# Kernel optimization log

Hardware: AMD Instinct MI355X
Metric: run time of the kernel (lower is better)

## Reference

```python
import jax, jax.numpy as jnp
import numpy as np

EPS = 1e-5

def _conv(x, w, b):
    # NCHW, OIHW, stride 1, SAME padding (kernel 3, padding 1)
    y = jax.lax.conv_general_dilated(x, w, (1, 1), 'SAME',
                                     dimension_numbers=('NCHW', 'OIHW', 'NCHW'))
    return y + b[None, :, None, None]

def _maxpool2(x):
    return jax.lax.reduce_window(x, -jnp.inf, jax.lax.max,
                                 (1, 1, 2, 2), (1, 1, 2, 2), 'VALID')

def _fraud_layer(v, theta, phases, sq_r, disp_r, disp_phi, kerr):
    # classical shim of a 2-mode photonic layer; all params are zero -> identity
    c, s = jnp.cos(theta), jnp.sin(theta)
    rot = jnp.array([[1.0, 0.0], [0.0, 1.0]]) * c + jnp.array([[0.0, -1.0], [1.0, 0.0]]) * s
    v = v @ rot.T
    v = v * jnp.cos(phases)          # phase shifters
    v = v * jnp.exp(sq_r)            # squeezing
    v = v + disp_r * jnp.cos(disp_phi)  # displacement
    return v + kerr * v ** 3         # Kerr nonlinearity

def setup_inputs() -> dict:
    key = jax.random.key(0)
    ks = jax.random.split(key, 16)
    B = 4096
    inp = {
        'x': jax.random.normal(ks[0], (B, 1, 32, 32), jnp.float32),
        'conv1_w': jax.random.normal(ks[1], (8, 1, 3, 3), jnp.float32) * 0.2,
        'conv1_b': jnp.zeros((8,), jnp.float32),
        'conv2_w': jax.random.normal(ks[2], (16, 8, 3, 3), jnp.float32) * 0.1,
        'conv2_b': jnp.zeros((16,), jnp.float32),
        'conv3_w': jax.random.normal(ks[3], (32, 16, 3, 3), jnp.float32) * 0.1,
        'conv3_b': jnp.zeros((32,), jnp.float32),
        'gnn_w1': jax.random.normal(ks[4], (32, 32), jnp.float32) * 0.2,
        'gnn_w2': jax.random.normal(ks[5], (16, 32), jnp.float32) * 0.2,
        'rotation_params': jax.random.normal(ks[6], (4, 4), jnp.float32),
        'entangle_params': jax.random.normal(ks[7], (3,), jnp.float32),
        'reduce_w': jax.random.normal(ks[8], (2, 32), jnp.float32) * 0.2,
        'reduce_b': jnp.zeros((2,), jnp.float32),
        'cls_w': jax.random.normal(ks[9], (2, 2), jnp.float32) * 0.5,
        'cls_b': jnp.zeros((2,), jnp.float32),
        'bn_gamma': jnp.ones((2,), jnp.float32),
        'bn_beta': jnp.zeros((2,), jnp.float32),
    }
    return inp

def reference(x, conv1_w, conv1_b, conv2_w, conv2_b, conv3_w, conv3_b,
              gnn_w1, gnn_w2, rotation_params, entangle_params,
              reduce_w, reduce_b, cls_w, cls_b, bn_gamma, bn_beta):
    B = x.shape[0]
    # CNN feature extractor
    h = jax.nn.relu(_conv(x, conv1_w, conv1_b))
    h = _maxpool2(h)
    h = jax.nn.relu(_conv(h, conv2_w, conv2_b))
    h = _maxpool2(h)
    h = jax.nn.relu(_conv(h, conv3_w, conv3_b))
    feats = jnp.mean(h, axis=(2, 3))  # AdaptiveAvgPool2d((1,1)) -> (B, 32)
    # GNN feedforward (batched equivalent of the per-sample Python loop)
    a = jnp.tanh(feats @ gnn_w1.T)    # (B, 32)
    g = jnp.tanh(a @ gnn_w2.T)        # (B, 16)
    # Quantum-style self-attention (runs on detached numpy in original -> stop_gradient)
    d = g.shape[-1]
    q = (g.reshape(B, 4, 4) @ rotation_params).reshape(B, d)
    k = (g.reshape(B, 4, 4) @ rotation_params.T).reshape(B, d)
    temp = jnp.mean(jnp.cos(entangle_params))
    logits = (q @ k.T) * (temp / jnp.sqrt(jnp.asarray(d, jnp.float32)))  # (B, B)
    attn = jax.nn.softmax(logits, axis=-1) @ g                           # (B, 16)
    rep = jnp.concatenate([g, attn], axis=-1)                            # (B, 32)
    rep = jax.lax.stop_gradient(rep)  # numpy round-trip breaks the autograd graph
    # reduce -> fraud layers (all-zero params -> identity) -> classifier
    reduced = rep @ reduce_w.T + reduce_b  # (B, 2)
    z = jnp.zeros((2,), jnp.float32)
    for _ in range(2):  # input layer + 1 hidden layer, all-zero FraudLayerParameters
        reduced = _fraud_layer(reduced, 0.0, z, z, z, z, z)
    out = reduced @ cls_w.T + cls_b  # (B, 2)
    # BatchNorm1d(2) in training mode: batch stats, biased variance
    mu = jnp.mean(out, axis=0)
    var = jnp.mean((out - mu) ** 2, axis=0)
    out = bn_gamma * (out - mu) * jax.lax.rsqrt(var + EPS) + bn_beta
    return out
```

## Files before the change

kernel.cpp:

```cpp
#include <hip/hip_runtime.h>
#include <math.h>

#define LOG2E 1.4426950408889634f

typedef _Float16 h2v __attribute__((ext_vector_type(2)));
typedef _Float16 h4  __attribute__((ext_vector_type(4)));
typedef _Float16 h8  __attribute__((ext_vector_type(8)));
typedef float    f4  __attribute__((ext_vector_type(4)));

__device__ __forceinline__ h2v pk(float a, float b) {
    return __builtin_bit_cast(h2v, __builtin_amdgcn_cvt_pkrtz(a, b));
}

__device__ __forceinline__ f4 mfma16x32(h8 a, h8 b, f4 c) {
    return __builtin_amdgcn_mfma_f32_16x16x32_f16(a, b, c, 0, 0, 0);
}

__device__ __forceinline__ f4 mfma16x16(h4 a, h4 b, f4 c) {
    return __builtin_amdgcn_mfma_f32_16x16x16f16(a, b, c, 0, 0, 0);
}

__device__ __forceinline__ float fast_tanh(float x) {
    const float xc = fminf(fmaxf(x, -15.f), 15.f);
    const float t = exp2f(xc * (2.f * LOG2E));
    return (t - 1.f) * __builtin_amdgcn_rcpf(t + 1.f);
}

__global__ __launch_bounds__(256) void k_pack(
    const float* __restrict__ w1,
    const float* __restrict__ w2, const float* __restrict__ w3,
    const float* __restrict__ ent,
    _Float16* __restrict__ w2f, _Float16* __restrict__ w3f,
    h2v* __restrict__ w1p, float* __restrict__ w1t,
    float* __restrict__ tsc)
{
    if (threadIdx.x == 0) {
        const float temp = (cosf(ent[0]) + cosf(ent[1]) + cosf(ent[2])) * (1.f / 3.f);
        tsc[0] = temp * 0.25f;
    }
    if (threadIdx.x < 24) {
        const int oc = threadIdx.x / 3, ky = threadIdx.x % 3;
        w1p[threadIdx.x] = pk(w1[oc * 9 + ky * 3 + 0], w1[oc * 9 + ky * 3 + 1]);
        w1t[threadIdx.x] = w1[oc * 9 + ky * 3 + 2];
    }
    for (int idx = threadIdx.x; idx < 1536; idx += 256) {
        const int j = idx & 7;
        const int lane = (idx >> 3) & 63;
        const int c = idx >> 9;
        const int oc = lane & 15;
        const int s = c * 4 + (lane >> 4);
        w2f[idx] = (s < 9) ? (_Float16)w2[oc * 72 + j * 9 + s] : (_Float16)0.f;
    }
    for (int idx = threadIdx.x; idx < 5120; idx += 256) {
        const int j = idx & 7;
        const int lane = (idx >> 3) & 63;
        const int rest = idx >> 9;
        const int mt = rest / 5;
        const int oc = mt * 16 + (lane & 15);
        const int kk = (lane >> 4) * 8 + j;
        const int ic = kk & 15;
        const int sh = (rest - mt * 5) * 2 + (kk >> 4);
        w3f[idx] = (sh < 9) ? (_Float16)w3[oc * 144 + ic * 9 + sh] : (_Float16)0.f;
    }
}

__global__ __launch_bounds__(256) void k_cnn(
    const float* __restrict__ x,
    const h2v* __restrict__ w1p, const float* __restrict__ w1t,
    const float* __restrict__ b1,
    const _Float16* __restrict__ w2f, const float* __restrict__ b2,
    const _Float16* __restrict__ w3f, const float* __restrict__ b3,
    const float* __restrict__ gw1,
    const float* __restrict__ gw2,
    const float* __restrict__ rot,
    const float* __restrict__ tsc,
    _Float16* __restrict__ q16, _Float16* __restrict__ k16,
    _Float16* __restrict__ g16, _Float16* __restrict__ gswz)
{
    __shared__ __align__(16) char smem[4624 + 5184 + 3200 + 256];
    float* xs   = (float*)smem;
    h8*  p1c    = (h8*)(smem + 4624);
    h8*  p2hc   = (h8*)(smem + 4624 + 5184);
    h4*  p2h4   = (h4*)(smem + 4624 + 5184);
    float* fsum = (float*)(smem + 4624 + 5184 + 3200);

    const int t = threadIdx.x;
    const int b = blockIdx.x;
    const int lane = t & 63;
    const int w = __builtin_amdgcn_readfirstlane(t >> 6);
    const int nn = lane & 15;
    const int kq = lane >> 4;

    const h8 hzero = (h8)(_Float16)0.f;
    const f4 fzero = {0.f, 0.f, 0.f, 0.f};

    const float4 v = ((const float4*)(x + (size_t)b * 1024))[t];

    if (t < 132) {
        int r, c;
        if (t < 34)       { r = 0;  c = t; }
        else if (t < 68)  { r = 33; c = t - 34; }
        else if (t < 100) { r = t - 68 + 1;  c = 0; }
        else              { r = t - 100 + 1; c = 33; }
        xs[r * 34 + c] = 0.f;
    } else if (t < 200) {
        const int u = t - 132;
        int r, c;
        if (u < 18)      { r = 0;  c = u; }
        else if (u < 36) { r = 17; c = u - 18; }
        else if (u < 52) { r = u - 36 + 1; c = 0; }
        else             { r = u - 52 + 1; c = 17; }
        p1c[r * 18 + c] = hzero;
    } else if (t < 236) {
        const int u = t - 200;
        int r, c;
        if (u < 10)      { r = 0; c = u; }
        else if (u < 20) { r = 9; c = u - 10; }
        else if (u < 28) { r = u - 20 + 1; c = 0; }
        else             { r = u - 28 + 1; c = 9; }
        p2hc[(r * 10 + c) * 2 + 0] = hzero;
        p2hc[(r * 10 + c) * 2 + 1] = hzero;
    }
    {
        const int row = t >> 3;
        const int col = (t & 7) << 2;
        float* dst = &xs[(row + 1) * 34 + col + 1];
        dst[0] = v.x; dst[1] = v.y; dst[2] = v.z; dst[3] = v.w;
    }
    __syncthreads();

    {
        const int px = t & 15, py = t >> 4;
        float pa[4][4];
        #pragma unroll
        for (int iy = 0; iy < 4; ++iy)
            #pragma unroll
            for (int ix = 0; ix < 4; ++ix)
                pa[iy][ix] = xs[(2 * py + iy) * 34 + (2 * px + ix)];
        h2v pA[4], pB[4];
        #pragma unroll
        for (int r = 0; r < 4; ++r) {
            pA[r] = pk(pa[r][0], pa[r][1]);
            pB[r] = pk(pa[r][1], pa[r][2]);
        }

        float r8[8];
        #pragma unroll
        for (int oc = 0; oc < 8; ++oc) {
            const h2v wp0 = w1p[oc * 3 + 0], wp1 = w1p[oc * 3 + 1], wp2 = w1p[oc * 3 + 2];
            const float wt0 = w1t[oc * 3 + 0], wt1 = w1t[oc * 3 + 1], wt2 = w1t[oc * 3 + 2];
            const float bb = b1[oc];
            float mx = -1e30f;
            #pragma unroll
            for (int sy = 0; sy < 2; ++sy) {
                float s0 = bb, s1 = bb;
                s0 = __builtin_amdgcn_fdot2(pA[sy],     wp0, s0, false);
                s0 = __builtin_amdgcn_fdot2(pA[sy + 1], wp1, s0, false);
                s0 = __builtin_amdgcn_fdot2(pA[sy + 2], wp2, s0, false);
                s0 = fmaf(pa[sy][2], wt0, s0);
                s0 = fmaf(pa[sy + 1][2], wt1, s0);
                s0 = fmaf(pa[sy + 2][2], wt2, s0);
                s1 = __builtin_amdgcn_fdot2(pB[sy],     wp0, s1, false);
                s1 = __builtin_amdgcn_fdot2(pB[sy + 1], wp1, s1, false);
                s1 = __builtin_amdgcn_fdot2(pB[sy + 2], wp2, s1, false);
                s1 = fmaf(pa[sy][3], wt0, s1);
                s1 = fmaf(pa[sy + 1][3], wt1, s1);
                s1 = fmaf(pa[sy + 2][3], wt2, s1);
                mx = fmaxf(mx, fmaxf(s0, s1));
            }
            r8[oc] = fmaxf(mx, 0.f);
        }
        union { h8 v; h2v p[4]; } u;
        #pragma unroll
        for (int ocp = 0; ocp < 4; ++ocp) u.p[ocp] = pk(r8[2 * ocp], r8[2 * ocp + 1]);
        p1c[(py + 1) * 18 + (px + 1)] = u.v;
    }

    h8 a2[3];
    #pragma unroll
    for (int c = 0; c < 3; ++c) a2[c] = ((const h8*)w2f)[c * 64 + lane];

    __syncthreads();

    f4 accp[4] = {fzero, fzero, fzero, fzero};
    #pragma unroll
    for (int c = 0; c < 3; ++c) {
        const int s = c * 4 + kq;
        const int ky = (s < 9) ? s / 3 : 0;
        const int kx = (s < 9) ? s % 3 : 0;
        #pragma unroll
        for (int p = 0; p < 4; ++p) {
            h8 bf = hzero;
            if (s < 9) bf = p1c[(4 * w + p + ky) * 18 + (nn + kx)];
            accp[p] = mfma16x32(a2[c], bf, accp[p]);
        }
    }

    {
        float bq[4];
        #pragma unroll
        for (int r = 0; r < 4; ++r) bq[r] = b2[kq * 4 + r];
        #pragma unroll
        for (int i = 0; i < 2; ++i) {
            float m2[4];
            #pragma unroll
            for (int r = 0; r < 4; ++r) {
                const float v0 = fmaxf(accp[2 * i][r] + bq[r], 0.f);
                const float v1 = fmaxf(accp[2 * i + 1][r] + bq[r], 0.f);
                float mv = fmaxf(v0, v1);
                mv = fmaxf(mv, __shfl_xor(mv, 1));
                m2[r] = mv;
            }
            if ((lane & 1) == 0) {
                const int px = nn >> 1;
                const int py = 2 * w + i;
                union { h4 v; h2v p[2]; } u;
                u.p[0] = pk(m2[0], m2[1]);
                u.p[1] = pk(m2[2], m2[3]);
                p2h4[((py + 1) * 10 + (px + 1)) * 4 + kq] = u.v;
            }
        }
    }

    const int mt = w >> 1;
    const int nt0 = (w & 1) * 2;
    h8 a3[5];
    #pragma unroll
    for (int c = 0; c < 5; ++c) a3[c] = ((const h8*)w3f)[(mt * 5 + c) * 64 + lane];

    __syncthreads();

    f4 acc3[2] = {fzero, fzero};
    #pragma unroll
    for (int c = 0; c < 5; ++c) {
        const int shv = 2 * c + (kq >> 1);
        const int hh = kq & 1;
        const int ky = (shv < 9) ? ((shv * 11) >> 5) : 0;
        const int kx = (shv < 9) ? (shv - 3 * ky) : 0;
        #pragma unroll
        for (int p = 0; p < 2; ++p) {
            const int pos = (nt0 + p) * 16 + nn;
            const int yy = pos >> 3, xx = pos & 7;
            h8 bf = hzero;
            if (shv < 9) bf = p2hc[((yy + ky) * 10 + (xx + kx)) * 2 + hh];
            acc3[p] = mfma16x32(a3[c], bf, acc3[p]);
        }
    }

    {
        float bq[4];
        #pragma unroll
        for (int r = 0; r < 4; ++r) bq[r] = b3[mt * 16 + kq * 4 + r];
        float sv[4];
        #pragma unroll
        for (int r = 0; r < 4; ++r) {
            float s = fmaxf(acc3[0][r] + bq[r], 0.f) + fmaxf(acc3[1][r] + bq[r], 0.f);
            #pragma unroll
            for (int off = 1; off < 16; off <<= 1) s += __shfl_xor(s, off);
            sv[r] = s;
        }
        if (nn == 0) {
            const f4 pack = {sv[0], sv[1], sv[2], sv[3]};
            ((f4*)fsum)[mt * 8 + (w & 1) * 4 + kq] = pack;
        }
    }
    __syncthreads();

    if (w != 0) return;

    const float qscale = tsc[0];

    const int l = t;
    const int i5 = l & 31;
    const float fsv = (fsum[(i5 >> 4) * 32 + (i5 & 15)] +
                       fsum[(i5 >> 4) * 32 + 16 + (i5 & 15)]) * (1.f / 64.f);

    float asv;
    {
        const int h = l >> 5;
        float s = 0.f;
        #pragma unroll
        for (int q4 = 0; q4 < 4; ++q4) {
            const float4 wv = ((const float4*)gw1)[i5 * 8 + h * 4 + q4];
            s = fmaf(wv.x, __shfl(fsv, h * 16 + q4 * 4 + 0), s);
            s = fmaf(wv.y, __shfl(fsv, h * 16 + q4 * 4 + 1), s);
            s = fmaf(wv.z, __shfl(fsv, h * 16 + q4 * 4 + 2), s);
            s = fmaf(wv.w, __shfl(fsv, h * 16 + q4 * 4 + 3), s);
        }
        s += __shfl_xor(s, 32);
        asv = fast_tanh(s);
    }

    const int i4 = l & 15;
    float gsv;
    {
        const int h = l >> 4;
        float s = 0.f;
        #pragma unroll
        for (int q4 = 0; q4 < 2; ++q4) {
            const float4 wv = ((const float4*)gw2)[i4 * 8 + h * 2 + q4];
            s = fmaf(wv.x, __shfl(asv, h * 8 + q4 * 4 + 0), s);
            s = fmaf(wv.y, __shfl(asv, h * 8 + q4 * 4 + 1), s);
            s = fmaf(wv.z, __shfl(asv, h * 8 + q4 * 4 + 2), s);
            s = fmaf(wv.w, __shfl(asv, h * 8 + q4 * 4 + 3), s);
        }
        s += __shfl_xor(s, 16);
        s += __shfl_xor(s, 32);
        gsv = fast_tanh(s);
    }

    const int grp = l >> 4;
    const int r = i4 >> 2, c = i4 & 3;
    float gq[4];
    #pragma unroll
    for (int j = 0; j < 4; ++j) gq[j] = __shfl(gsv, r * 4 + j);

    float v2;
    if (grp == 0) {
        v2 = 0.f;
        #pragma unroll
        for (int j = 0; j < 4; ++j) v2 = fmaf(gq[j], rot[j * 4 + c], v2);
        v2 *= qscale;
    } else if (grp == 1) {
        v2 = 0.f;
        #pragma unroll
        for (int j = 0; j < 4; ++j) v2 = fmaf(gq[j], rot[c * 4 + j], v2);
    } else {
        v2 = gsv;
    }
    const float vn = __shfl_xor(v2, 1);

    if (grp == 3) {
        const int tile = b >> 4, lc = b & 15;
        gswz[tile * 256 + (((lc >> 2) * 16) + i4) * 4 + (lc & 3)] = (_Float16)gsv;
    } else if ((i4 & 1) == 0) {
        const h2v pv = pk(v2, vn);
        if (grp == 0)      ((h2v*)q16)[b * 8 + (i4 >> 1)] = pv;
        else if (grp == 1) ((h2v*)k16)[b * 8 + (i4 >> 1)] = pv;
        else               ((h2v*)g16)[b * 8 + (i4 >> 1)] = pv;
    }
}

__global__ __launch_bounds__(1024) void k_attn(
    const _Float16* __restrict__ q16, const _Float16* __restrict__ k16,
    const _Float16* __restrict__ g16, const _Float16* __restrict__ gswz,
    const float* __restrict__ rw, const float* __restrict__ rb,
    const float* __restrict__ cw, const float* __restrict__ cb,
    float* __restrict__ outp, int B)
{
    __shared__ f4 lO[16][64];
    __shared__ float lm[16][16];
    __shared__ float ll[16][16];

    const int t = threadIdx.x;
    const int lane = t & 63;
    const int w = t >> 6;
    const int rt = blockIdx.x;
    const int r = lane & 15;
    const int q = lane >> 4;
    const f4 fzero = {0.f, 0.f, 0.f, 0.f};

    const h4 qf = *(const h4*)(q16 + ((size_t)(rt * 16 + r)) * 16 + q * 4);

    float m = -1e30f, lp = 0.f;
    f4 O = fzero;

    const int strip = B >> 4;
    const int cbeg = w * strip;

    h4 kf = *(const h4*)(k16 + ((size_t)(cbeg + r)) * 16 + q * 4);
    h4 gf = *(const h4*)(gswz + (size_t)(cbeg >> 4) * 256 + lane * 4);

    for (int ci = 0; ci < strip; ci += 16) {
        const int cnext = (ci + 16 < strip) ? (cbeg + ci + 16) : cbeg;
        const h4 kf_n = *(const h4*)(k16 + ((size_t)(cnext + r)) * 16 + q * 4);
        const h4 gf_n = *(const h4*)(gswz + (size_t)(cnext >> 4) * 256 + lane * 4);

        const f4 st = mfma16x16(kf, qf, fzero);

        float mx = fmaxf(fmaxf(st[0], st[1]), fmaxf(st[2], st[3]));
        mx = fmaxf(mx, __shfl_xor(mx, 16));
        mx = fmaxf(mx, __shfl_xor(mx, 32));
        if (__ballot(mx > m)) {
            const float mn = fmaxf(m, mx);
            const float a = exp2f((m - mn) * LOG2E);
            lp *= a;
            O[0] *= a; O[1] *= a; O[2] *= a; O[3] *= a;
            m = mn;
        }
        const float p0 = exp2f((st[0] - m) * LOG2E);
        const float p1 = exp2f((st[1] - m) * LOG2E);
        const float p2 = exp2f((st[2] - m) * LOG2E);
        const float p3 = exp2f((st[3] - m) * LOG2E);
        lp += (p0 + p1) + (p2 + p3);

        union { h4 v; h2v p[2]; } u;
        u.p[0] = pk(p0, p1);
        u.p[1] = pk(p2, p3);
        O = mfma16x16(gf, u.v, O);

        kf = kf_n;
        gf = gf_n;
    }
    lp += __shfl_xor(lp, 16);
    lp += __shfl_xor(lp, 32);

    lO[w][lane] = O;
    if (lane < 16) { lm[w][lane] = m; ll[w][lane] = lp; }
    __syncthreads();

    if (w == 0) {
        float M = lm[0][r];
        #pragma unroll
        for (int ww = 1; ww < 16; ++ww) M = fmaxf(M, lm[ww][r]);
        float L = 0.f;
        f4 Om = fzero;
        #pragma unroll
        for (int ww = 0; ww < 16; ++ww) {
            const float f = exp2f((lm[ww][r] - M) * LOG2E);
            L = fmaf(ll[ww][r], f, L);
            const f4 ow = lO[ww][lane];
            Om[0] = fmaf(ow[0], f, Om[0]);
            Om[1] = fmaf(ow[1], f, Om[1]);
            Om[2] = fmaf(ow[2], f, Om[2]);
            Om[3] = fmaf(ow[3], f, Om[3]);
        }
        const float il = 1.f / L;
        const h4 gr = *(const h4*)(g16 + ((size_t)(rt * 16 + r)) * 16 + q * 4);

        float rv[2];
        #pragma unroll
        for (int c = 0; c < 2; ++c) {
            float s = 0.f;
            #pragma unroll
            for (int j = 0; j < 4; ++j) {
                s = fmaf((float)gr[j], rw[c * 32 + q * 4 + j], s);
                s = fmaf(Om[j] * il, rw[c * 32 + 16 + q * 4 + j], s);
            }
            s += __shfl_xor(s, 16);
            s += __shfl_xor(s, 32);
            rv[c] = s + rb[c];
        }
        if (q == 0) {
            float2 o;
            o.x = cb[0] + cw[0] * rv[0] + cw[1] * rv[1];
            o.y = cb[1] + cw[2] * rv[0] + cw[3] * rv[1];
            ((float2*)outp)[rt * 16 + r] = o;
        }
    }
}

__global__ __launch_bounds__(1024) void k_bn(
    float* __restrict__ data, const float* __restrict__ gamma,
    const float* __restrict__ beta, int B)
{
    __shared__ float red[16][4];
    __shared__ float coef[4];
    const int t = threadIdx.x;
    float s0 = 0.f, s1 = 0.f, q0 = 0.f, q1 = 0.f;
    for (int i = t; i < B; i += 1024) {
        const float2 v = ((const float2*)data)[i];
        s0 += v.x; q0 += v.x * v.x;
        s1 += v.y; q1 += v.y * v.y;
    }
    #pragma unroll
    for (int off = 32; off; off >>= 1) {
        s0 += __shfl_xor(s0, off); q0 += __shfl_xor(q0, off);
        s1 += __shfl_xor(s1, off); q1 += __shfl_xor(q1, off);
    }
    if ((t & 63) == 0) {
        red[t >> 6][0] = s0; red[t >> 6][1] = q0;
        red[t >> 6][2] = s1; red[t >> 6][3] = q1;
    }
    __syncthreads();
    if (t == 0) {
        float S0 = 0.f, Q0 = 0.f, S1 = 0.f, Q1 = 0.f;
        for (int w = 0; w < 16; ++w) {
            S0 += red[w][0]; Q0 += red[w][1]; S1 += red[w][2]; Q1 += red[w][3];
        }
        const float inv = 1.f / (float)B;
        const float mu0 = S0 * inv, mu1 = S1 * inv;
        const float v0 = Q0 * inv - mu0 * mu0;
        const float v1 = Q1 * inv - mu1 * mu1;
        const float sc0 = gamma[0] * rsqrtf(v0 + 1e-5f);
        const float sc1 = gamma[1] * rsqrtf(v1 + 1e-5f);
        coef[0] = sc0; coef[1] = beta[0] - mu0 * sc0;
        coef[2] = sc1; coef[3] = beta[1] - mu1 * sc1;
    }
    __syncthreads();
    const float sc0 = coef[0], sh0 = coef[1], sc1 = coef[2], sh1 = coef[3];
    for (int i = t; i < B; i += 1024) {
        float2 v = ((const float2*)data)[i];
        v.x = fmaf(v.x, sc0, sh0);
        v.y = fmaf(v.y, sc1, sh1);
        ((float2*)data)[i] = v;
    }
}

extern "C" void kernel_launch(void* const* d_in, const int* in_sizes, int n_in,
                              void* d_out, int out_size, void* d_ws, size_t ws_size,
                              hipStream_t stream)
{
    (void)n_in; (void)out_size; (void)ws_size;
    const float* x   = (const float*)d_in[0];
    const float* w1  = (const float*)d_in[1];
    const float* b1  = (const float*)d_in[2];
    const float* w2  = (const float*)d_in[3];
    const float* b2  = (const float*)d_in[4];
    const float* w3  = (const float*)d_in[5];
    const float* b3  = (const float*)d_in[6];
    const float* gw1 = (const float*)d_in[7];
    const float* gw2 = (const float*)d_in[8];
    const float* rot = (const float*)d_in[9];
    const float* ent = (const float*)d_in[10];
    const float* rw  = (const float*)d_in[11];
    const float* rbv = (const float*)d_in[12];
    const float* cw  = (const float*)d_in[13];
    const float* cbv = (const float*)d_in[14];
    const float* gam = (const float*)d_in[15];
    const float* bet = (const float*)d_in[16];

    const int B = in_sizes[0] / (32 * 32);

    _Float16* q16  = (_Float16*)d_ws;
    _Float16* k16  = q16 + (size_t)B * 16;
    _Float16* g16  = k16 + (size_t)B * 16;
    _Float16* gswz = g16 + (size_t)B * 16;
    _Float16* w2f  = gswz + (size_t)B * 16;
    _Float16* w3f  = w2f + 1536;
    h2v*      w1p  = (h2v*)(w3f + 5120);
    float*    w1t  = (float*)(w1p + 24);
    float*    tsc  = w1t + 24;
    float* pre = (float*)d_out;

    k_pack<<<1, 256, 0, stream>>>(w1, w2, w3, ent, w2f, w3f, w1p, w1t, tsc);
    k_cnn<<<B, 256, 0, stream>>>(x, w1p, w1t, b1, w2f, b2, w3f, b3, gw1, gw2,
                                 rot, tsc, q16, k16, g16, gswz);
    k_attn<<<B / 16, 1024, 0, stream>>>(q16, k16, g16, gswz, rw, rbv, cw, cbv,
                                        pre, B);
    k_bn<<<1, 1024, 0, stream>>>(pre, gam, bet, B);
}
```

Measured before the change: 133.8 us.

## Accumulate BatchNorm statistics in attention kernel and deepen K/G prefetch

The attention kernel now reduces each tile's output sums and squared sums with shuffles and adds them to a global accumulator with atomics. The BN kernel then only reads these totals instead of re-scanning the whole output to compute mean and variance. Separately, the attention loop prefetches K and G fragments two tiles ahead instead of one, to hide more load latency. Float atomics make the reduction order nondeterministic, and the deeper prefetch costs extra registers.

```diff
diff --git a/kernel.cpp b/kernel.cpp
--- a/kernel.cpp
+++ b/kernel.cpp
@@ -32,12 +32,13 @@
     const float* __restrict__ ent,
     _Float16* __restrict__ w2f, _Float16* __restrict__ w3f,
     h2v* __restrict__ w1p, float* __restrict__ w1t,
-    float* __restrict__ tsc)
+    float* __restrict__ tsc, float* __restrict__ bnacc)
 {
     if (threadIdx.x == 0) {
         const float temp = (cosf(ent[0]) + cosf(ent[1]) + cosf(ent[2])) * (1.f / 3.f);
         tsc[0] = temp * 0.25f;
     }
+    if (threadIdx.x < 4) bnacc[threadIdx.x] = 0.f;
     if (threadIdx.x < 24) {
         const int oc = threadIdx.x / 3, ky = threadIdx.x % 3;
         w1p[threadIdx.x] = pk(w1[oc * 9 + ky * 3 + 0], w1[oc * 9 + ky * 3 + 1]);
@@ -346,7 +347,7 @@
     const _Float16* __restrict__ g16, const _Float16* __restrict__ gswz,
     const float* __restrict__ rw, const float* __restrict__ rb,
     const float* __restrict__ cw, const float* __restrict__ cb,
-    float* __restrict__ outp, int B)
+    float* __restrict__ outp, float* __restrict__ bnacc, int B)
 {
     __shared__ f4 lO[16][64];
     __shared__ float lm[16][16];
@@ -368,15 +369,17 @@
     const int strip = B >> 4;
     const int cbeg = w * strip;
 
-    h4 kf = *(const h4*)(k16 + ((size_t)(cbeg + r)) * 16 + q * 4);
-    h4 gf = *(const h4*)(gswz + (size_t)(cbeg >> 4) * 256 + lane * 4);
+    h4 kfA = *(const h4*)(k16 + ((size_t)(cbeg + r)) * 16 + q * 4);
+    h4 gfA = *(const h4*)(gswz + (size_t)(cbeg >> 4) * 256 + lane * 4);
+    h4 kfB = *(const h4*)(k16 + ((size_t)(cbeg + 16 + r)) * 16 + q * 4);
+    h4 gfB = *(const h4*)(gswz + (size_t)((cbeg + 16) >> 4) * 256 + lane * 4);
 
     for (int ci = 0; ci < strip; ci += 16) {
-        const int cnext = (ci + 16 < strip) ? (cbeg + ci + 16) : cbeg;
-        const h4 kf_n = *(const h4*)(k16 + ((size_t)(cnext + r)) * 16 + q * 4);
-        const h4 gf_n = *(const h4*)(gswz + (size_t)(cnext >> 4) * 256 + lane * 4);
-
-        const f4 st = mfma16x16(kf, qf, fzero);
+        const int cn = (ci + 32 < strip) ? (cbeg + ci + 32) : cbeg;
+        const h4 kfC = *(const h4*)(k16 + ((size_t)(cn + r)) * 16 + q * 4);
+        const h4 gfC = *(const h4*)(gswz + (size_t)(cn >> 4) * 256 + lane * 4);
+
+        const f4 st = mfma16x16(kfA, qf, fzero);
 
         float mx = fmaxf(fmaxf(st[0], st[1]), fmaxf(st[2], st[3]));
         mx = fmaxf(mx, __shfl_xor(mx, 16));
@@ -397,10 +400,10 @@
         union { h4 v; h2v p[2]; } u;
         u.p[0] = pk(p0, p1);
         u.p[1] = pk(p2, p3);
-        O = mfma16x16(gf, u.v, O);
-
-        kf = kf_n;
-        gf = gf_n;
+        O = mfma16x16(gfA, u.v, O);
+
+        kfA = kfB; gfA = gfB;
+        kfB = kfC; gfB = gfC;
     }
     lp += __shfl_xor(lp, 16);
     lp += __shfl_xor(lp, 32);
@@ -446,42 +449,34 @@
             o.x = cb[0] + cw[0] * rv[0] + cw[1] * rv[1];
             o.y = cb[1] + cw[2] * rv[0] + cw[3] * rv[1];
             ((float2*)outp)[rt * 16 + r] = o;
+
+            float s0 = o.x, s1 = o.y, q0 = o.x * o.x, q1 = o.y * o.y;
+            #pragma unroll
+            for (int off = 1; off < 16; off <<= 1) {
+                s0 += __shfl_xor(s0, off); q0 += __shfl_xor(q0, off);
+                s1 += __shfl_xor(s1, off); q1 += __shfl_xor(q1, off);
+            }
+            if (r == 0) {
+                atomicAdd(bnacc + 0, s0);
+                atomicAdd(bnacc + 1, q0);
+                atomicAdd(bnacc + 2, s1);
+                atomicAdd(bnacc + 3, q1);
+            }
         }
     }
 }
 
 __global__ __launch_bounds__(1024) void k_bn(
-    float* __restrict__ data, const float* __restrict__ gamma,
-    const float* __restrict__ beta, int B)
+    float* __restrict__ data, const float* __restrict__ bnacc,
+    const float* __restrict__ gamma, const float* __restrict__ beta, int B)
 {
-    __shared__ float red[16][4];
     __shared__ float coef[4];
     const int t = threadIdx.x;
-    float s0 = 0.f, s1 = 0.f, q0 = 0.f, q1 = 0.f;
-    for (int i = t; i < B; i += 1024) {
-        const float2 v = ((const float2*)data)[i];
-        s0 += v.x; q0 += v.x * v.x;
-        s1 += v.y; q1 += v.y * v.y;
-    }
-    #pragma unroll
-    for (int off = 32; off; off >>= 1) {
-        s0 += __shfl_xor(s0, off); q0 += __shfl_xor(q0, off);
-        s1 += __shfl_xor(s1, off); q1 += __shfl_xor(q1, off);
-    }
-    if ((t & 63) == 0) {
-        red[t >> 6][0] = s0; red[t >> 6][1] = q0;
-        red[t >> 6][2] = s1; red[t >> 6][3] = q1;
-    }
-    __syncthreads();
     if (t == 0) {
-        float S0 = 0.f, Q0 = 0.f, S1 = 0.f, Q1 = 0.f;
-        for (int w = 0; w < 16; ++w) {
-            S0 += red[w][0]; Q0 += red[w][1]; S1 += red[w][2]; Q1 += red[w][3];
-        }
         const float inv = 1.f / (float)B;
-        const float mu0 = S0 * inv, mu1 = S1 * inv;
-        const float v0 = Q0 * inv - mu0 * mu0;
-        const float v1 = Q1 * inv - mu1 * mu1;
+        const float mu0 = bnacc[0] * inv, mu1 = bnacc[2] * inv;
+        const float v0 = bnacc[1] * inv - mu0 * mu0;
+        const float v1 = bnacc[3] * inv - mu1 * mu1;
         const float sc0 = gamma[0] * rsqrtf(v0 + 1e-5f);
         const float sc1 = gamma[1] * rsqrtf(v1 + 1e-5f);
         coef[0] = sc0; coef[1] = beta[0] - mu0 * sc0;
@@ -531,12 +526,13 @@
     h2v*      w1p  = (h2v*)(w3f + 5120);
     float*    w1t  = (float*)(w1p + 24);
     float*    tsc  = w1t + 24;
+    float*    bnacc = tsc + 1;
     float* pre = (float*)d_out;
 
-    k_pack<<<1, 256, 0, stream>>>(w1, w2, w3, ent, w2f, w3f, w1p, w1t, tsc);
+    k_pack<<<1, 256, 0, stream>>>(w1, w2, w3, ent, w2f, w3f, w1p, w1t, tsc, bnacc);
     k_cnn<<<B, 256, 0, stream>>>(x, w1p, w1t, b1, w2f, b2, w3f, b3, gw1, gw2,
                                  rot, tsc, q16, k16, g16, gswz);
     k_attn<<<B / 16, 1024, 0, stream>>>(q16, k16, g16, gswz, rw, rbv, cw, cbv,
-                                        pre, B);
-    k_bn<<<1, 1024, 0, stream>>>(pre, gam, bet, B);
-}
+                                        pre, bnacc, B);
+    k_bn<<<1, 1024, 0, stream>>>(pre, bnacc, gam, bet, B);
+}
```

New measurement: 145.7 us. 1.09x slower.
